# Kernel tuning notes

Hardware: AMD Instinct MI355X
Metric: run time of the kernel (lower is better)

## Reference

```python
import jax, jax.numpy as jnp
import numpy as np
from functools import partial

IMAGE_SIZE = 256
ORIG_SIZE = 1024
NEAR, FAR = 0.1, 100.0
CHUNK = 100  # faces processed per scan step to bound memory


def setup_inputs():
    key = jax.random.key(0)
    kv, kf = jax.random.split(key)
    B, V, F = 4, 5000, 10000
    verts = jax.random.normal(kv, (B, V, 3), jnp.float32) * 0.4
    verts = verts.at[..., 2].add(2.5)  # object in front of camera (+z)
    faces = jax.random.randint(kf, (B, F, 3), 0, V)
    fx = fy = float(ORIG_SIZE)
    cx = cy = ORIG_SIZE / 2.0
    K = jnp.broadcast_to(jnp.array([[fx, 0., cx], [0., fy, cy], [0., 0., 1.]], jnp.float32), (B, 3, 3))
    R = jnp.broadcast_to(jnp.eye(3, dtype=jnp.float32), (B, 3, 3))
    t = jnp.zeros((B, 1, 3), jnp.float32)
    dist_coeffs = jnp.zeros((B, 5), jnp.float32)
    return {"vertices": verts, "faces": faces, "K": K, "R": R, "t": t, "dist_coeffs": dist_coeffs}


def projection(vertices, K, R, t, dist_coeffs, orig_size, eps=1e-9):
    # vertices: [B,V,3]; matmul(vertices, R^T) + t, OpenCV distortion, intrinsics, NDC
    v = jnp.einsum('bvj,bij->bvi', vertices, R) + t
    x, y, z = v[..., 0], v[..., 1], v[..., 2]
    x_ = x / (z + eps)
    y_ = y / (z + eps)
    k1, k2, p1, p2, k3 = [dist_coeffs[:, i:i + 1] for i in range(5)]
    r2 = x_ * x_ + y_ * y_
    rad = 1. + k1 * r2 + k2 * r2 * r2 + k3 * r2 * r2 * r2
    x__ = x_ * rad + 2. * p1 * x_ * y_ + p2 * (r2 + 2. * x_ * x_)
    y__ = y_ * rad + p1 * (r2 + 2. * y_ * y_) + 2. * p2 * x_ * y_
    vv = jnp.stack([x__, y__, jnp.ones_like(z)], axis=-1)
    vv = jnp.einsum('bvj,bij->bvi', vv, K)
    u, vc = vv[..., 0], vv[..., 1]
    vc = orig_size - vc  # image y points down
    u = 2. * (u - orig_size / 2.) / orig_size
    vc = 2. * (vc - orig_size / 2.) / orig_size
    return jnp.stack([u, vc, z], axis=-1)  # [B,V,3] in NDC xy, camera z


def vertices_to_faces(vertices, faces):
    # vertices [B,V,3], faces [B,F,3] -> [B,F,3,3]
    return jnp.take_along_axis(vertices[:, :, None, :], faces[:, :, :, None], axis=1)


def rasterize_depth(face_verts, image_size, near, far):
    # face_verts: [B,F,3,3]; z-buffer min of barycentric-interpolated 1/z depth
    B, F = face_verts.shape[:2]
    pad = (-F) % CHUNK
    fv = jnp.pad(face_verts, ((0, 0), (0, pad), (0, 0), (0, 0)))  # padded faces are degenerate
    n_chunks = (F + pad) // CHUNK
    fv = fv.reshape(B, n_chunks, CHUNK, 3, 3).transpose(1, 0, 2, 3, 4)  # [n,B,C,3,3]
    ps = (2. * jnp.arange(image_size, dtype=jnp.float32) + 1. - image_size) / image_size
    xp = ps[None, None, None, :]  # [1,1,1,W]
    yp = ps[None, None, :, None]  # [1,1,H,1]
    eps = 1e-8

    def step(zbuf, chunk):  # chunk [B,C,3,3]
        x = chunk[..., 0]
        y = chunk[..., 1]
        z = chunk[..., 2]
        x0, x1, x2 = (x[..., i, None, None] for i in range(3))
        y0, y1, y2 = (y[..., i, None, None] for i in range(3))
        z0, z1, z2 = (z[..., i, None, None] for i in range(3))
        denom = (y1 - y2) * (x0 - x2) + (x2 - x1) * (y0 - y2)
        ok = jnp.abs(denom) > eps
        safe_d = jnp.where(ok, denom, 1.)
        w0 = ((y1 - y2) * (xp - x2) + (x2 - x1) * (yp - y2)) / safe_d  # [B,C,H,W]
        w1 = ((y2 - y0) * (xp - x2) + (x0 - x2) * (yp - y2)) / safe_d
        w2 = 1. - w0 - w1
        inside = (w0 >= 0.) & (w1 >= 0.) & (w2 >= 0.) & ok
        zs0 = jnp.where(z0 > eps, z0, 1.)
        zs1 = jnp.where(z1 > eps, z1, 1.)
        zs2 = jnp.where(z2 > eps, z2, 1.)
        zinv = w0 / zs0 + w1 / zs1 + w2 / zs2
        zp = 1. / jnp.where(zinv > eps, zinv, 1.)
        valid = inside & (zp > near) & (zp < far) & (z0 > eps) & (z1 > eps) & (z2 > eps)
        zp = jnp.where(valid, zp, far)
        zbuf = jnp.minimum(zbuf, jnp.min(zp, axis=1))  # min over faces in chunk
        return zbuf, None

    zbuf0 = jnp.full((B, image_size, image_size), far, dtype=face_verts.dtype)
    zbuf, _ = jax.lax.scan(step, zbuf0, fv)
    return zbuf[:, ::-1, :]  # flip vertically to image convention


def reference(vertices, faces, K, R, t, dist_coeffs):
    # fill_back: append faces with reversed winding
    faces_fb = jnp.concatenate([faces, faces[:, :, ::-1]], axis=1)
    v_ndc = projection(vertices, K, R, t, dist_coeffs, float(ORIG_SIZE))
    fverts = vertices_to_faces(v_ndc, faces_fb)  # [B,2F,3,3]
    return rasterize_depth(fverts, IMAGE_SIZE, NEAR, FAR)  # [B,H,W] depth map
```

## Files before the change

kernel.cpp:

```cpp
#include <hip/hip_runtime.h>

#define IMG 256
#define TW 32
#define TH 32
#define TXN (IMG/TW)
#define TYN (IMG/TH)
#define TILES (TXN*TYN)
#define SUBSPLIT 16
#define BIGF 1e30f

typedef float v4f __attribute__((ext_vector_type(4)));

__device__ __forceinline__ float ndc(int i) { return (2.0f*i + 1.0f - IMG) * (1.0f/IMG); }

__device__ __forceinline__ void rank_to_tile(int rank, int& tx, int& ty) {
    int k, base;
    if (rank < 4)       { k = 0; base = 0;  }
    else if (rank < 16) { k = 1; base = 4;  }
    else if (rank < 36) { k = 2; base = 16; }
    else                { k = 3; base = 36; }
    int j = rank - base;
    int s = 2*k + 2;
    int seg = j / (s - 1);
    int off = j - seg * (s - 1);
    int lo = 3 - k, hi = 4 + k;
    if      (seg == 0) { tx = lo + off; ty = lo; }
    else if (seg == 1) { tx = hi;       ty = lo + off; }
    else if (seg == 2) { tx = hi - off; ty = hi; }
    else               { tx = lo;       ty = hi - off; }
}

__global__ void k_prep(const float* __restrict__ verts, const int* __restrict__ faces,
                       const float* __restrict__ Km, const float* __restrict__ Rm,
                       const float* __restrict__ tm, const float* __restrict__ dm,
                       v4f* __restrict__ fd, v4f* __restrict__ bb,
                       unsigned int* __restrict__ outz,
                       int B, int V, int F, int nz, int faceBlocks) {
    if ((int)blockIdx.x >= faceBlocks) {
        int idx = (blockIdx.x - faceBlocks) * 256 + threadIdx.x;
        int stride = (gridDim.x - faceBlocks) * 256;
        for (int j = idx; j < nz; j += stride) outz[j] = 0x42C80000u;
        return;
    }
    int i = blockIdx.x * 256 + threadIdx.x;
    if (i >= B * F) return;
    int b = i / F;
    const float* vb = verts + (size_t)b * V * 3;
    const float* R = Rm + b * 9;
    const float* K = Km + b * 9;
    const float* t = tm + b * 3;
    const float* d = dm + b * 5;
    float X[3], Y[3], Z[3];
    #pragma unroll
    for (int c = 0; c < 3; ++c) {
        int vi = faces[3*i + c];
        float px = vb[3*vi], py = vb[3*vi+1], pz = vb[3*vi+2];
        float x = R[0]*px + R[1]*py + R[2]*pz + t[0];
        float y = R[3]*px + R[4]*py + R[5]*pz + t[1];
        float z = R[6]*px + R[7]*py + R[8]*pz + t[2];
        float iz = 1.0f / (z + 1e-9f);
        float x_ = x * iz, y_ = y * iz;
        float k1 = d[0], k2 = d[1], p1 = d[2], p2 = d[3], k3 = d[4];
        float r2 = x_*x_ + y_*y_;
        float rad = 1.0f + k1*r2 + k2*r2*r2 + k3*r2*r2*r2;
        float xd = x_*rad + 2.0f*p1*x_*y_ + p2*(r2 + 2.0f*x_*x_);
        float yd = y_*rad + p1*(r2 + 2.0f*y_*y_) + 2.0f*p2*x_*y_;
        float u  = K[0]*xd + K[1]*yd + K[2];
        float vc = K[3]*xd + K[4]*yd + K[5];
        vc = 1024.0f - vc;
        X[c] = (u  - 512.0f) * (1.0f/512.0f);
        Y[c] = (vc - 512.0f) * (1.0f/512.0f);
        Z[c] = z;
    }
    float x0=X[0], y0=Y[0], z0=Z[0], x1=X[1], y1=Y[1], z1=Z[1], x2=X[2], y2=Y[2], z2=Z[2];
    float denom = (y1-y2)*(x0-x2) + (x2-x1)*(y0-y2);
    bool ok = (fabsf(denom) > 1e-8f) && (z0 > 1e-8f) && (z1 > 1e-8f) && (z2 > 1e-8f);
    if (!ok) { bb[i] = (v4f){3e38f, -3e38f, 3e38f, -3e38f}; return; }
    float s = (denom > 0.0f) ? 1.0f : -1.0f;
    float absd = fabsf(denom);
    float P0x = s*(y1-y2), P0y = s*(x2-x1);
    float P1x = s*(y2-y0), P1y = s*(x0-x2);
    float P2x = -(P0x + P1x), P2y = -(P0y + P1y);
    float A0 = -(P0x*x2 + P0y*y2);
    float A1 = -(P1x*x2 + P1y*y2);
    float A2 = absd - A0 - A1;
    float ia  = 1.0f / absd;
    float rz0 = ia / z0, rz1 = ia / z1, rz2 = ia / z2;
    float zix = P0x*rz0 + P1x*rz1 + P2x*rz2;
    float ziy = P0y*rz0 + P1y*rz1 + P2y*rz2;
    float zic = A0*rz0 + A1*rz1 + A2*rz2;
    fd[(size_t)i*3 + 0] = (v4f){P0x, P1x, P2x, -zix};
    fd[(size_t)i*3 + 1] = (v4f){P0y, P1y, P2y, -ziy};
    fd[(size_t)i*3 + 2] = (v4f){A0,  A1,  A2,  10.0f - zic};
    bb[i] = (v4f){fminf(x0, fminf(x1, x2)) - 1e-4f,
                  fmaxf(x0, fmaxf(x1, x2)) + 1e-4f,
                  fminf(y0, fminf(y1, y2)) - 1e-4f,
                  fmaxf(y0, fmaxf(y1, y2)) + 1e-4f};
}

__device__ __forceinline__ bool tile_test(v4f gx, v4f gy, v4f a,
                                          float txlo, float txhi, float tylo, float tyhi) {
    float m0 = fmaxf(gx.x*txlo, gx.x*txhi) + fmaxf(gy.x*tylo, gy.x*tyhi) + a.x;
    float m1 = fmaxf(gx.y*txlo, gx.y*txhi) + fmaxf(gy.y*tylo, gy.y*tyhi) + a.y;
    float m2 = fmaxf(gx.z*txlo, gx.z*txhi) + fmaxf(gy.z*tylo, gy.z*tyhi) + a.z;
    return fminf(fminf(m0, m1), m2) >= -1e-5f;
}

__device__ __forceinline__ float plane_min(float gw, float hw, float aw,
                                           float xlo, float xhi, float ylo, float yhi) {
    return fminf(gw*xlo, gw*xhi) + fminf(hw*ylo, hw*yhi) + aw;
}

__device__ __forceinline__ float wave_max_dpp(float v) {
    int x;
    x = __builtin_amdgcn_update_dpp(0, __float_as_int(v), 0x111, 0xF, 0xF, true);
    v = fmaxf(v, __int_as_float(x));
    x = __builtin_amdgcn_update_dpp(0, __float_as_int(v), 0x112, 0xF, 0xF, true);
    v = fmaxf(v, __int_as_float(x));
    x = __builtin_amdgcn_update_dpp(0, __float_as_int(v), 0x114, 0xF, 0xF, true);
    v = fmaxf(v, __int_as_float(x));
    x = __builtin_amdgcn_update_dpp(0, __float_as_int(v), 0x118, 0xF, 0xF, true);
    v = fmaxf(v, __int_as_float(x));
    x = __builtin_amdgcn_update_dpp(0, __float_as_int(v), 0x142, 0xF, 0xF, true);
    v = fmaxf(v, __int_as_float(x));
    x = __builtin_amdgcn_update_dpp(0, __float_as_int(v), 0x143, 0xF, 0xF, true);
    v = fmaxf(v, __int_as_float(x));
    return __int_as_float(__builtin_amdgcn_readlane(__float_as_int(v), 63));
}

__global__ __launch_bounds__(256) void k_raster(const v4f* __restrict__ fd,
                                                const v4f* __restrict__ bb,
                                                unsigned int* __restrict__ outz,
                                                int B, int F) {
    __shared__ v4f sA[257], sB[257], sC[257];
    int tid = threadIdx.x, lane = tid & 63, wave = tid >> 6;
    int wbase = wave << 6;
    int j = blockIdx.x >> 4;
    int s = blockIdx.x & (SUBSPLIT-1);
    int nTB = TILES * B;
    int f_begin = (s * F) / SUBSPLIT, f_end = ((s + 1) * F) / SUBSPLIT;

    #pragma unroll 1
    for (int phase = 0; phase < 2; ++phase) {
        int tb = (phase == 0) ? j : (nTB - 1 - j);
        int rank = tb / B;
        int b = tb - rank * B;
        int tx, ty;
        rank_to_tile(rank, tx, ty);
        int rowbase = ty*TH + wave*8;
        int row = rowbase + (lane >> 3);
        int col = tx*TW + (lane & 7) * 4;
        float yp = ndc(row);
        float xp[4];
        #pragma unroll
        for (int jj = 0; jj < 4; ++jj) xp[jj] = ndc(col + jj);
        float txlo = ndc(tx*TW), txhi = ndc(tx*TW + TW - 1);
        float bylo = ndc(rowbase), byhi = ndc(rowbase + 7);
        float m[4] = {BIGF, BIGF, BIGF, BIGF};
        float h = 9.99f;

        const v4f* bbp = bb + (size_t)b * F;
        const v4f* fdp = fd + (size_t)b * F * 3;

        v4f box = bbp[min(f_begin + lane, f_end - 1)];
        bool valid = (f_begin + lane) < f_end;

        for (int g0 = f_begin; g0 < f_end; g0 += 64) {
            int fn = g0 + 64 + lane;
            v4f nbox = bbp[min(fn, f_end - 1)];
            bool nvalid = fn < f_end;

            bool pass = valid &
                        (box.x <= txhi) & (box.y >= txlo) &
                        (box.z <= byhi) & (box.w >= bylo);
            v4f ra, rb, rc;
            if (pass) {
                int f = g0 + lane;
                ra = fdp[3*f]; rb = fdp[3*f+1]; rc = fdp[3*f+2];
                pass = tile_test(ra, rb, rc, txlo, txhi, bylo, byhi)
                    && (plane_min(ra.w, rb.w, rc.w, txlo, txhi, bylo, byhi) < h);
            }
            unsigned long long mk = __ballot(pass);
            int total = __popcll(mk);
            if (pass) {
                int slot = wbase + __popcll(mk & ((1ull << lane) - 1ull));
                sA[slot] = ra;
                sB[slot] = rb;
                sC[slot] = rc;
            }
            if (total > 0) {
                v4f gx = sA[wbase], gy = sB[wbase], aa = sC[wbase];
                for (int i = 0; i < total; ++i) {
                    v4f nx = sA[wbase+i+1], ny = sB[wbase+i+1], nzv = sC[wbase+i+1];
                    float e0 = fmaf(gy.x, yp, aa.x);
                    float e1 = fmaf(gy.y, yp, aa.y);
                    float e2 = fmaf(gy.z, yp, aa.z);
                    float e3 = fmaf(gy.w, yp, aa.w);
                    #pragma unroll
                    for (int jj = 0; jj < 4; ++jj) {
                        float n0 = fmaf(gx.x, xp[jj], e0);
                        float n1 = fmaf(gx.y, xp[jj], e1);
                        float n2 = fmaf(gx.z, xp[jj], e2);
                        float n3 = fmaf(gx.w, xp[jj], e3);
                        float q = fminf(fminf(n0, n1), n2);
                        m[jj] = fminf(m[jj], (q >= 0.0f) ? n3 : BIGF);
                    }
                    gx = nx; gy = ny; aa = nzv;
                }
                h = fminf(9.99f, wave_max_dpp(fmaxf(fmaxf(m[0], m[1]), fmaxf(m[2], m[3]))));
            }
            box = nbox; valid = nvalid;
        }
        int orow = IMG - 1 - row;
        size_t zo = (size_t)b * (IMG*IMG) + (size_t)orow * IMG + col;
        #pragma unroll
        for (int jj = 0; jj < 4; ++jj) {
            if (m[jj] < 9.99f) {
                float depth = 1.0f / (10.0f - m[jj]);
                unsigned int mv = __float_as_uint(depth);
                unsigned int cv = outz[zo + jj];
                if (mv < cv) atomicMin(&outz[zo + jj], mv);
            }
        }
    }
}

__global__ __launch_bounds__(256) void k_brute(const v4f* __restrict__ fd,
                                               const v4f* __restrict__ bb,
                                               float* __restrict__ out, int B, int F) {
    int bid = blockIdx.x;
    int stripe = bid % 64, b = bid / 64;
    int tid = threadIdx.x, lane = tid & 63, wave = tid >> 6;
    int row = stripe * 4 + wave, colb = lane * 4;
    float yp = ndc(row);
    float xp[4]; float m[4];
    #pragma unroll
    for (int j = 0; j < 4; ++j) { xp[j] = ndc(colb + j); m[j] = BIGF; }
    const v4f* fbb = bb + (size_t)b * F;
    const v4f* ffd = fd + (size_t)b * F * 3;
    for (int f = 0; f < F; ++f) {
        v4f box = fbb[f];
        if (box.z > yp || box.w < yp) continue;
        v4f gx = ffd[3*f], gy = ffd[3*f+1], aa = ffd[3*f+2];
        float e0 = fmaf(gy.x, yp, aa.x);
        float e1 = fmaf(gy.y, yp, aa.y);
        float e2 = fmaf(gy.z, yp, aa.z);
        float e3 = fmaf(gy.w, yp, aa.w);
        #pragma unroll
        for (int j = 0; j < 4; ++j) {
            float n0 = fmaf(gx.x, xp[j], e0);
            float n1 = fmaf(gx.y, xp[j], e1);
            float n2 = fmaf(gx.z, xp[j], e2);
            float n3 = fmaf(gx.w, xp[j], e3);
            float mn = fminf(fminf(fminf(n0, n1), n2), n3);
            m[j] = fminf(m[j], (mn >= 0.0f) ? n3 : BIGF);
        }
    }
    size_t o = (size_t)b*(IMG*IMG) + (size_t)(IMG-1-row)*IMG + colb;
    float4 r;
    r.x = (m[0] < 9.99f) ? 1.0f/(10.0f-m[0]) : 100.0f;
    r.y = (m[1] < 9.99f) ? 1.0f/(10.0f-m[1]) : 100.0f;
    r.z = (m[2] < 9.99f) ? 1.0f/(10.0f-m[2]) : 100.0f;
    r.w = (m[3] < 9.99f) ? 1.0f/(10.0f-m[3]) : 100.0f;
    *(float4*)(out + o) = r;
}

extern "C" void kernel_launch(void* const* d_in, const int* in_sizes, int n_in,
                              void* d_out, int out_size, void* d_ws, size_t ws_size,
                              hipStream_t stream) {
    const float* verts = (const float*)d_in[0];
    const int*   faces = (const int*)d_in[1];
    const float* Km    = (const float*)d_in[2];
    const float* Rm    = (const float*)d_in[3];
    const float* tm    = (const float*)d_in[4];
    const float* dm    = (const float*)d_in[5];
    float* out = (float*)d_out;

    int B = in_sizes[2] / 9;
    int V = in_sizes[0] / (3 * B);
    int F = in_sizes[1] / (3 * B);
    int nz = B * IMG * IMG;

    char* ws = (char*)d_ws;
    size_t al = 255;
    size_t o_fd  = 0;
    size_t o_bb  = (o_fd + (size_t)B*F*48 + al) & ~al;
    size_t need  = o_bb + (size_t)B*F*16;

    v4f* fd  = (v4f*)(ws + o_fd);
    v4f* bbp = (v4f*)(ws + o_bb);

    const int thr = 256;
    int faceBlocks = (B*F + thr - 1) / thr;
    int rasterBlocks = (TILES * B / 2) * SUBSPLIT;
    if (ws_size >= need) {
        k_prep<<<faceBlocks + 128, thr, 0, stream>>>(verts, faces, Km, Rm, tm, dm,
                                                     fd, bbp, (unsigned int*)out,
                                                     B, V, F, nz, faceBlocks);
        k_raster<<<rasterBlocks, thr, 0, stream>>>(fd, bbp, (unsigned int*)out, B, F);
    }
}
```

Before: 139.6 us.

## Use atomic work-ticket queue per wave over tile-band-split items, unroll face loop by two

Replaces the static block-to-tile mapping, where four waves each took one 8-row band of a tile and two phases paired tiles, with a persistent-style dynamic scheduler. Each wave grabs an item (tile, batch, face-split, row band) through a global atomic ticket, so waves balance independently of one another. The face-evaluation inner loop is also unrolled by two, using a sentinel padding entry that can never pass the inside test. This targets load imbalance between center and edge tiles, at the cost of one atomic per item and a ticket reset in the prep kernel.

Result: slower. 363.3 us (+160.1%).

```diff
diff --git a/kernel.cpp b/kernel.cpp
--- a/kernel.cpp
+++ b/kernel.cpp
@@ -34,9 +34,10 @@
                        const float* __restrict__ Km, const float* __restrict__ Rm,
                        const float* __restrict__ tm, const float* __restrict__ dm,
                        v4f* __restrict__ fd, v4f* __restrict__ bb,
-                       unsigned int* __restrict__ outz,
+                       unsigned int* __restrict__ outz, unsigned int* __restrict__ ticket,
                        int B, int V, int F, int nz, int faceBlocks) {
     if ((int)blockIdx.x >= faceBlocks) {
+        if ((int)blockIdx.x == faceBlocks && threadIdx.x == 0) *ticket = 0u;
         int idx = (blockIdx.x - faceBlocks) * 256 + threadIdx.x;
         int stride = (gridDim.x - faceBlocks) * 256;
         for (int j = idx; j < nz; j += stride) outz[j] = 0x42C80000u;
@@ -128,26 +129,46 @@
     return __int_as_float(__builtin_amdgcn_readlane(__float_as_int(v), 63));
 }
 
+#define EVAL_FACE(gx, gy, aa)                                        \
+    {                                                                \
+        float e0 = fmaf((gy).x, yp, (aa).x);                         \
+        float e1 = fmaf((gy).y, yp, (aa).y);                         \
+        float e2 = fmaf((gy).z, yp, (aa).z);                         \
+        float e3 = fmaf((gy).w, yp, (aa).w);                         \
+        _Pragma("unroll")                                            \
+        for (int jj = 0; jj < 4; ++jj) {                             \
+            float n0 = fmaf((gx).x, xp[jj], e0);                     \
+            float n1 = fmaf((gx).y, xp[jj], e1);                     \
+            float n2 = fmaf((gx).z, xp[jj], e2);                     \
+            float n3 = fmaf((gx).w, xp[jj], e3);                     \
+            float q = fminf(fminf(n0, n1), n2);                      \
+            m[jj] = fminf(m[jj], (q >= 0.0f) ? n3 : BIGF);           \
+        }                                                            \
+    }
+
 __global__ __launch_bounds__(256) void k_raster(const v4f* __restrict__ fd,
                                                 const v4f* __restrict__ bb,
                                                 unsigned int* __restrict__ outz,
-                                                int B, int F) {
-    __shared__ v4f sA[257], sB[257], sC[257];
+                                                unsigned int* __restrict__ ticket,
+                                                int B, int F, int nItems) {
+    __shared__ v4f sA[260], sB[260], sC[260];
     int tid = threadIdx.x, lane = tid & 63, wave = tid >> 6;
     int wbase = wave << 6;
-    int j = blockIdx.x >> 4;
-    int s = blockIdx.x & (SUBSPLIT-1);
-    int nTB = TILES * B;
-    int f_begin = (s * F) / SUBSPLIT, f_end = ((s + 1) * F) / SUBSPLIT;
-
-    #pragma unroll 1
-    for (int phase = 0; phase < 2; ++phase) {
-        int tb = (phase == 0) ? j : (nTB - 1 - j);
+
+    for (;;) {
+        int it = 0;
+        if (lane == 0) it = (int)atomicAdd(ticket, 1u);
+        it = __builtin_amdgcn_readfirstlane(it);
+        if (it >= nItems) break;
+
+        int band = it & 3;
+        int sIdx = (it >> 2) & (SUBSPLIT - 1);
+        int tb   = it >> 6;
         int rank = tb / B;
         int b = tb - rank * B;
         int tx, ty;
         rank_to_tile(rank, tx, ty);
-        int rowbase = ty*TH + wave*8;
+        int rowbase = ty*TH + band*8;
         int row = rowbase + (lane >> 3);
         int col = tx*TW + (lane & 7) * 4;
         float yp = ndc(row);
@@ -159,6 +180,7 @@
         float m[4] = {BIGF, BIGF, BIGF, BIGF};
         float h = 9.99f;
 
+        int f_begin = (sIdx * F) / SUBSPLIT, f_end = ((sIdx + 1) * F) / SUBSPLIT;
         const v4f* bbp = bb + (size_t)b * F;
         const v4f* fdp = fd + (size_t)b * F * 3;
 
@@ -189,23 +211,20 @@
                 sC[slot] = rc;
             }
             if (total > 0) {
-                v4f gx = sA[wbase], gy = sB[wbase], aa = sC[wbase];
-                for (int i = 0; i < total; ++i) {
-                    v4f nx = sA[wbase+i+1], ny = sB[wbase+i+1], nzv = sC[wbase+i+1];
-                    float e0 = fmaf(gy.x, yp, aa.x);
-                    float e1 = fmaf(gy.y, yp, aa.y);
-                    float e2 = fmaf(gy.z, yp, aa.z);
-                    float e3 = fmaf(gy.w, yp, aa.w);
-                    #pragma unroll
-                    for (int jj = 0; jj < 4; ++jj) {
-                        float n0 = fmaf(gx.x, xp[jj], e0);
-                        float n1 = fmaf(gx.y, xp[jj], e1);
-                        float n2 = fmaf(gx.z, xp[jj], e2);
-                        float n3 = fmaf(gx.w, xp[jj], e3);
-                        float q = fminf(fminf(n0, n1), n2);
-                        m[jj] = fminf(m[jj], (q >= 0.0f) ? n3 : BIGF);
-                    }
-                    gx = nx; gy = ny; aa = nzv;
+                if (lane == 0) {
+                    sA[wbase+total] = (v4f){0.0f, 0.0f, 0.0f, 0.0f};
+                    sB[wbase+total] = (v4f){0.0f, 0.0f, 0.0f, 0.0f};
+                    sC[wbase+total] = (v4f){-1.0f, -1.0f, -1.0f, 0.0f};
+                }
+                v4f gx0 = sA[wbase+0], gy0 = sB[wbase+0], aa0 = sC[wbase+0];
+                v4f gx1 = sA[wbase+1], gy1 = sB[wbase+1], aa1 = sC[wbase+1];
+                for (int i = 0; i < total; i += 2) {
+                    v4f px0 = sA[wbase+i+2], py0 = sB[wbase+i+2], pa0 = sC[wbase+i+2];
+                    v4f px1 = sA[wbase+i+3], py1 = sB[wbase+i+3], pa1 = sC[wbase+i+3];
+                    EVAL_FACE(gx0, gy0, aa0);
+                    EVAL_FACE(gx1, gy1, aa1);
+                    gx0 = px0; gy0 = py0; aa0 = pa0;
+                    gx1 = px1; gy1 = py1; aa1 = pa1;
                 }
                 h = fminf(9.99f, wave_max_dpp(fmaxf(fmaxf(m[0], m[1]), fmaxf(m[2], m[3]))));
             }
@@ -285,18 +304,22 @@
     size_t al = 255;
     size_t o_fd  = 0;
     size_t o_bb  = (o_fd + (size_t)B*F*48 + al) & ~al;
-    size_t need  = o_bb + (size_t)B*F*16;
+    size_t o_tk  = (o_bb + (size_t)B*F*16 + al) & ~al;
+    size_t need  = o_tk + 256;
 
     v4f* fd  = (v4f*)(ws + o_fd);
     v4f* bbp = (v4f*)(ws + o_bb);
+    unsigned int* ticket = (unsigned int*)(ws + o_tk);
 
     const int thr = 256;
     int faceBlocks = (B*F + thr - 1) / thr;
-    int rasterBlocks = (TILES * B / 2) * SUBSPLIT;
+    int nItems = TILES * B * SUBSPLIT * 4;
+    int rasterBlocks = 2048;
     if (ws_size >= need) {
         k_prep<<<faceBlocks + 128, thr, 0, stream>>>(verts, faces, Km, Rm, tm, dm,
-                                                     fd, bbp, (unsigned int*)out,
+                                                     fd, bbp, (unsigned int*)out, ticket,
                                                      B, V, F, nz, faceBlocks);
-        k_raster<<<rasterBlocks, thr, 0, stream>>>(fd, bbp, (unsigned int*)out, B, F);
-    }
-}
+        k_raster<<<rasterBlocks, thr, 0, stream>>>(fd, bbp, (unsigned int*)out, ticket,
+                                                   B, F, nItems);
+    }
+}
```

## Bin faces into per-tile lists before rasterizing instead of scanning all faces

Applied to the files above, without the earlier changes.

Adds a binning pipeline in place of scanning every face per tile. k_prep computes a per-face tile coverage mask and per-bin counts, k_scan builds prefix offsets, and k_fill writes face ids into per-(tile,batch) lists. k_raster then walks only its bin's ids, split across the subsplit blocks. This removes the cost of each tile iterating over all faces, at the price of three extra launches, a memset, a second coverage computation, atomics, and indirect gathers through the id list. The old full-scan raster is kept as a fallback when the workspace is too small.

Result: slower. 157.6 us (+12.8%).

```diff
diff --git a/kernel.cpp b/kernel.cpp
--- a/kernel.cpp
+++ b/kernel.cpp
@@ -3,9 +3,9 @@
 #define IMG 256
 #define TW 32
 #define TH 32
-#define TXN (IMG/TW)
-#define TYN (IMG/TH)
-#define TILES (TXN*TYN)
+#define TXN 8
+#define TYN 8
+#define TILES 64
 #define SUBSPLIT 16
 #define BIGF 1e30f
 
@@ -30,74 +30,6 @@
     else               { tx = lo;       ty = hi - off; }
 }
 
-__global__ void k_prep(const float* __restrict__ verts, const int* __restrict__ faces,
-                       const float* __restrict__ Km, const float* __restrict__ Rm,
-                       const float* __restrict__ tm, const float* __restrict__ dm,
-                       v4f* __restrict__ fd, v4f* __restrict__ bb,
-                       unsigned int* __restrict__ outz,
-                       int B, int V, int F, int nz, int faceBlocks) {
-    if ((int)blockIdx.x >= faceBlocks) {
-        int idx = (blockIdx.x - faceBlocks) * 256 + threadIdx.x;
-        int stride = (gridDim.x - faceBlocks) * 256;
-        for (int j = idx; j < nz; j += stride) outz[j] = 0x42C80000u;
-        return;
-    }
-    int i = blockIdx.x * 256 + threadIdx.x;
-    if (i >= B * F) return;
-    int b = i / F;
-    const float* vb = verts + (size_t)b * V * 3;
-    const float* R = Rm + b * 9;
-    const float* K = Km + b * 9;
-    const float* t = tm + b * 3;
-    const float* d = dm + b * 5;
-    float X[3], Y[3], Z[3];
-    #pragma unroll
-    for (int c = 0; c < 3; ++c) {
-        int vi = faces[3*i + c];
-        float px = vb[3*vi], py = vb[3*vi+1], pz = vb[3*vi+2];
-        float x = R[0]*px + R[1]*py + R[2]*pz + t[0];
-        float y = R[3]*px + R[4]*py + R[5]*pz + t[1];
-        float z = R[6]*px + R[7]*py + R[8]*pz + t[2];
-        float iz = 1.0f / (z + 1e-9f);
-        float x_ = x * iz, y_ = y * iz;
-        float k1 = d[0], k2 = d[1], p1 = d[2], p2 = d[3], k3 = d[4];
-        float r2 = x_*x_ + y_*y_;
-        float rad = 1.0f + k1*r2 + k2*r2*r2 + k3*r2*r2*r2;
-        float xd = x_*rad + 2.0f*p1*x_*y_ + p2*(r2 + 2.0f*x_*x_);
-        float yd = y_*rad + p1*(r2 + 2.0f*y_*y_) + 2.0f*p2*x_*y_;
-        float u  = K[0]*xd + K[1]*yd + K[2];
-        float vc = K[3]*xd + K[4]*yd + K[5];
-        vc = 1024.0f - vc;
-        X[c] = (u  - 512.0f) * (1.0f/512.0f);
-        Y[c] = (vc - 512.0f) * (1.0f/512.0f);
-        Z[c] = z;
-    }
-    float x0=X[0], y0=Y[0], z0=Z[0], x1=X[1], y1=Y[1], z1=Z[1], x2=X[2], y2=Y[2], z2=Z[2];
-    float denom = (y1-y2)*(x0-x2) + (x2-x1)*(y0-y2);
-    bool ok = (fabsf(denom) > 1e-8f) && (z0 > 1e-8f) && (z1 > 1e-8f) && (z2 > 1e-8f);
-    if (!ok) { bb[i] = (v4f){3e38f, -3e38f, 3e38f, -3e38f}; return; }
-    float s = (denom > 0.0f) ? 1.0f : -1.0f;
-    float absd = fabsf(denom);
-    float P0x = s*(y1-y2), P0y = s*(x2-x1);
-    float P1x = s*(y2-y0), P1y = s*(x0-x2);
-    float P2x = -(P0x + P1x), P2y = -(P0y + P1y);
-    float A0 = -(P0x*x2 + P0y*y2);
-    float A1 = -(P1x*x2 + P1y*y2);
-    float A2 = absd - A0 - A1;
-    float ia  = 1.0f / absd;
-    float rz0 = ia / z0, rz1 = ia / z1, rz2 = ia / z2;
-    float zix = P0x*rz0 + P1x*rz1 + P2x*rz2;
-    float ziy = P0y*rz0 + P1y*rz1 + P2y*rz2;
-    float zic = A0*rz0 + A1*rz1 + A2*rz2;
-    fd[(size_t)i*3 + 0] = (v4f){P0x, P1x, P2x, -zix};
-    fd[(size_t)i*3 + 1] = (v4f){P0y, P1y, P2y, -ziy};
-    fd[(size_t)i*3 + 2] = (v4f){A0,  A1,  A2,  10.0f - zic};
-    bb[i] = (v4f){fminf(x0, fminf(x1, x2)) - 1e-4f,
-                  fmaxf(x0, fmaxf(x1, x2)) + 1e-4f,
-                  fminf(y0, fminf(y1, y2)) - 1e-4f,
-                  fmaxf(y0, fmaxf(y1, y2)) + 1e-4f};
-}
-
 __device__ __forceinline__ bool tile_test(v4f gx, v4f gy, v4f a,
                                           float txlo, float txhi, float tylo, float tyhi) {
     float m0 = fmaxf(gx.x*txlo, gx.x*txhi) + fmaxf(gy.x*tylo, gy.x*tyhi) + a.x;
@@ -128,10 +60,303 @@
     return __int_as_float(__builtin_amdgcn_readlane(__float_as_int(v), 63));
 }
 
+__device__ __forceinline__ unsigned long long cover_mask(float xmn, float xmx,
+                                                         float ymn, float ymx,
+                                                         v4f gx, v4f gy, v4f aa) {
+    int i0 = (int)floorf(xmn*128.0f + 127.5f);
+    int i1 = (int)ceilf (xmx*128.0f + 127.5f);
+    int j0 = (int)floorf(ymn*128.0f + 127.5f);
+    int j1 = (int)ceilf (ymx*128.0f + 127.5f);
+    if (i0 > 255 || i1 < 0 || j0 > 255 || j1 < 0) return 0ull;
+    int tx0 = max(i0, 0) >> 5, tx1 = min(i1, 255) >> 5;
+    int ty0 = max(j0, 0) >> 5, ty1 = min(j1, 255) >> 5;
+    unsigned long long m = 0ull;
+    for (int ty = ty0; ty <= ty1; ++ty) {
+        float tylo = ndc(ty*TH), tyhi = ndc(ty*TH + TH - 1);
+        for (int tx = tx0; tx <= tx1; ++tx) {
+            if (tile_test(gx, gy, aa, ndc(tx*TW), ndc(tx*TW + TW - 1), tylo, tyhi))
+                m |= 1ull << (ty*8 + tx);
+        }
+    }
+    return m;
+}
+
+__global__ void k_prep(const float* __restrict__ verts, const int* __restrict__ faces,
+                       const float* __restrict__ Km, const float* __restrict__ Rm,
+                       const float* __restrict__ tm, const float* __restrict__ dm,
+                       v4f* __restrict__ fd, v4f* __restrict__ bb,
+                       unsigned int* __restrict__ outz, unsigned int* __restrict__ gcnt,
+                       int B, int V, int F, int nz, int faceBlocks, int doBins) {
+    if ((int)blockIdx.x >= faceBlocks) {
+        int idx = (blockIdx.x - faceBlocks) * 256 + threadIdx.x;
+        int stride = (gridDim.x - faceBlocks) * 256;
+        for (int j = idx; j < nz; j += stride) outz[j] = 0x42C80000u;
+        return;
+    }
+    __shared__ int lcnt[1024];
+    int nbins = TILES * B;
+    int tid = threadIdx.x;
+    if (doBins) {
+        for (int k = tid; k < nbins; k += 256) lcnt[k] = 0;
+        __syncthreads();
+    }
+    int i = blockIdx.x * 256 + tid;
+    bool alive = i < B * F;
+    unsigned long long tmask = 0ull;
+    int b = 0;
+    if (alive) {
+        b = i / F;
+        const float* vb = verts + (size_t)b * V * 3;
+        const float* R = Rm + b * 9;
+        const float* K = Km + b * 9;
+        const float* t = tm + b * 3;
+        const float* d = dm + b * 5;
+        float X[3], Y[3], Z[3];
+        #pragma unroll
+        for (int c = 0; c < 3; ++c) {
+            int vi = faces[3*i + c];
+            float px = vb[3*vi], py = vb[3*vi+1], pz = vb[3*vi+2];
+            float x = R[0]*px + R[1]*py + R[2]*pz + t[0];
+            float y = R[3]*px + R[4]*py + R[5]*pz + t[1];
+            float z = R[6]*px + R[7]*py + R[8]*pz + t[2];
+            float iz = 1.0f / (z + 1e-9f);
+            float x_ = x * iz, y_ = y * iz;
+            float k1 = d[0], k2 = d[1], p1 = d[2], p2 = d[3], k3 = d[4];
+            float r2 = x_*x_ + y_*y_;
+            float rad = 1.0f + k1*r2 + k2*r2*r2 + k3*r2*r2*r2;
+            float xd = x_*rad + 2.0f*p1*x_*y_ + p2*(r2 + 2.0f*x_*x_);
+            float yd = y_*rad + p1*(r2 + 2.0f*y_*y_) + 2.0f*p2*x_*y_;
+            float u  = K[0]*xd + K[1]*yd + K[2];
+            float vc = K[3]*xd + K[4]*yd + K[5];
+            vc = 1024.0f - vc;
+            X[c] = (u  - 512.0f) * (1.0f/512.0f);
+            Y[c] = (vc - 512.0f) * (1.0f/512.0f);
+            Z[c] = z;
+        }
+        float x0=X[0], y0=Y[0], z0=Z[0], x1=X[1], y1=Y[1], z1=Z[1], x2=X[2], y2=Y[2], z2=Z[2];
+        float denom = (y1-y2)*(x0-x2) + (x2-x1)*(y0-y2);
+        bool ok = (fabsf(denom) > 1e-8f) && (z0 > 1e-8f) && (z1 > 1e-8f) && (z2 > 1e-8f);
+        if (!ok) {
+            bb[i] = (v4f){3e38f, -3e38f, 3e38f, -3e38f};
+        } else {
+            float s = (denom > 0.0f) ? 1.0f : -1.0f;
+            float absd = fabsf(denom);
+            float P0x = s*(y1-y2), P0y = s*(x2-x1);
+            float P1x = s*(y2-y0), P1y = s*(x0-x2);
+            float P2x = -(P0x + P1x), P2y = -(P0y + P1y);
+            float A0 = -(P0x*x2 + P0y*y2);
+            float A1 = -(P1x*x2 + P1y*y2);
+            float A2 = absd - A0 - A1;
+            float ia  = 1.0f / absd;
+            float rz0 = ia / z0, rz1 = ia / z1, rz2 = ia / z2;
+            float zix = P0x*rz0 + P1x*rz1 + P2x*rz2;
+            float ziy = P0y*rz0 + P1y*rz1 + P2y*rz2;
+            float zic = A0*rz0 + A1*rz1 + A2*rz2;
+            v4f ga = (v4f){P0x, P1x, P2x, -zix};
+            v4f gb = (v4f){P0y, P1y, P2y, -ziy};
+            v4f gc = (v4f){A0,  A1,  A2,  10.0f - zic};
+            fd[(size_t)i*3 + 0] = ga;
+            fd[(size_t)i*3 + 1] = gb;
+            fd[(size_t)i*3 + 2] = gc;
+            float xmn = fminf(x0, fminf(x1, x2)) - 1e-4f;
+            float xmx = fmaxf(x0, fmaxf(x1, x2)) + 1e-4f;
+            float ymn = fminf(y0, fminf(y1, y2)) - 1e-4f;
+            float ymx = fmaxf(y0, fmaxf(y1, y2)) + 1e-4f;
+            bb[i] = (v4f){xmn, xmx, ymn, ymx};
+            if (doBins) tmask = cover_mask(xmn, xmx, ymn, ymx, ga, gb, gc);
+        }
+    }
+    if (doBins) {
+        unsigned long long mk = tmask;
+        while (mk) {
+            int t = __builtin_ctzll(mk); mk &= mk - 1ull;
+            atomicAdd(&lcnt[t*B + b], 1);
+        }
+        __syncthreads();
+        for (int k = tid; k < nbins; k += 256)
+            if (lcnt[k]) atomicAdd(&gcnt[k], (unsigned int)lcnt[k]);
+    }
+}
+
+__global__ __launch_bounds__(256) void k_scan(const unsigned int* __restrict__ gcnt,
+                                              unsigned int* __restrict__ goff,
+                                              unsigned int* __restrict__ gcur, int nbins) {
+    __shared__ unsigned int ps[256];
+    int tid = threadIdx.x;
+    unsigned int loc[4], s = 0;
+    #pragma unroll
+    for (int k = 0; k < 4; ++k) {
+        int idx = tid*4 + k;
+        unsigned int c = (idx < nbins) ? gcnt[idx] : 0u;
+        loc[k] = c; s += c;
+    }
+    ps[tid] = s; __syncthreads();
+    #pragma unroll
+    for (int d = 1; d < 256; d <<= 1) {
+        unsigned int t = (tid >= d) ? ps[tid - d] : 0u;
+        __syncthreads();
+        ps[tid] += t;
+        __syncthreads();
+    }
+    unsigned int run = ps[tid] - s;
+    #pragma unroll
+    for (int k = 0; k < 4; ++k) {
+        int idx = tid*4 + k;
+        if (idx < nbins) {
+            goff[idx] = run; gcur[idx] = run; run += loc[k];
+            if (idx == nbins - 1) goff[nbins] = run;
+        }
+    }
+}
+
+__global__ void k_fill(const v4f* __restrict__ fd, const v4f* __restrict__ bb,
+                       unsigned int* __restrict__ gcur, unsigned int* __restrict__ ids,
+                       int B, int F) {
+    __shared__ int lcnt[1024];
+    __shared__ unsigned int lbase[1024];
+    __shared__ int lofs[1024];
+    int nbins = TILES * B;
+    int tid = threadIdx.x;
+    for (int k = tid; k < nbins; k += 256) { lcnt[k] = 0; lofs[k] = 0; }
+    __syncthreads();
+    int i = blockIdx.x * 256 + tid;
+    bool alive = i < B * F;
+    unsigned long long tmask = 0ull;
+    int b = 0;
+    if (alive) {
+        b = i / F;
+        v4f box = bb[i];
+        if (box.x <= box.y) {
+            v4f ga = fd[(size_t)i*3], gb = fd[(size_t)i*3+1], gc = fd[(size_t)i*3+2];
+            tmask = cover_mask(box.x, box.y, box.z, box.w, ga, gb, gc);
+        }
+    }
+    unsigned long long mk = tmask;
+    while (mk) {
+        int t = __builtin_ctzll(mk); mk &= mk - 1ull;
+        atomicAdd(&lcnt[t*B + b], 1);
+    }
+    __syncthreads();
+    for (int k = tid; k < nbins; k += 256)
+        if (lcnt[k]) lbase[k] = atomicAdd(&gcur[k], (unsigned int)lcnt[k]);
+    __syncthreads();
+    mk = tmask;
+    while (mk) {
+        int t = __builtin_ctzll(mk); mk &= mk - 1ull;
+        int bin = t*B + b;
+        int sl = atomicAdd(&lofs[bin], 1);
+        ids[lbase[bin] + sl] = (unsigned int)i;
+    }
+}
+
 __global__ __launch_bounds__(256) void k_raster(const v4f* __restrict__ fd,
                                                 const v4f* __restrict__ bb,
+                                                const unsigned int* __restrict__ ids,
+                                                const unsigned int* __restrict__ goff,
+                                                const unsigned int* __restrict__ gcnt,
                                                 unsigned int* __restrict__ outz,
                                                 int B, int F) {
+    __shared__ v4f sA[260], sB[260], sC[260];
+    int tid = threadIdx.x, lane = tid & 63, wave = tid >> 6;
+    int wbase = wave << 6;
+    int j = blockIdx.x >> 4;
+    int s = blockIdx.x & (SUBSPLIT-1);
+    int nTB = TILES * B;
+
+    #pragma unroll 1
+    for (int phase = 0; phase < 2; ++phase) {
+        int tb = (phase == 0) ? j : (nTB - 1 - j);
+        int rank = tb / B;
+        int b = tb - rank * B;
+        int tx, ty;
+        rank_to_tile(rank, tx, ty);
+        int bin = (ty*8 + tx)*B + b;
+        unsigned int off = goff[bin], len = gcnt[bin];
+        unsigned int p0 = off + (unsigned int)(( (unsigned long long)s    * len) / SUBSPLIT);
+        unsigned int p1 = off + (unsigned int)(( (unsigned long long)(s+1)* len) / SUBSPLIT);
+
+        int rowbase = ty*TH + wave*8;
+        int row = rowbase + (lane >> 3);
+        int col = tx*TW + (lane & 7) * 4;
+        float yp = ndc(row);
+        float xp[4];
+        #pragma unroll
+        for (int jj = 0; jj < 4; ++jj) xp[jj] = ndc(col + jj);
+        float txlo = ndc(tx*TW), txhi = ndc(tx*TW + TW - 1);
+        float bylo = ndc(rowbase), byhi = ndc(rowbase + 7);
+        float m[4] = {BIGF, BIGF, BIGF, BIGF};
+        float h = 9.99f;
+
+        if (p1 > p0) {
+            unsigned int idc = ids[min(p0 + lane, p1 - 1)];
+            bool vc = (p0 + lane) < p1;
+            v4f boxc = bb[idc];
+            unsigned int idn = ids[min(p0 + 64 + lane, p1 - 1)];
+            bool vn = (p0 + 64 + lane) < p1;
+
+            for (unsigned int p = p0; p < p1; p += 64) {
+                v4f boxn = bb[idn];
+                unsigned int id2 = ids[min(p + 128 + lane, p1 - 1)];
+                bool v2 = (p + 128 + lane) < p1;
+
+                bool pass = vc & (boxc.z <= byhi) & (boxc.w >= bylo);
+                v4f ra, rb, rc;
+                if (pass) {
+                    ra = fd[(size_t)idc*3]; rb = fd[(size_t)idc*3+1]; rc = fd[(size_t)idc*3+2];
+                    pass = tile_test(ra, rb, rc, txlo, txhi, bylo, byhi)
+                        && (plane_min(ra.w, rb.w, rc.w, txlo, txhi, bylo, byhi) < h);
+                }
+                unsigned long long mk = __ballot(pass);
+                int total = __popcll(mk);
+                if (pass) {
+                    int slot = wbase + __popcll(mk & ((1ull << lane) - 1ull));
+                    sA[slot] = ra;
+                    sB[slot] = rb;
+                    sC[slot] = rc;
+                }
+                if (total > 0) {
+                    v4f gx = sA[wbase], gy = sB[wbase], aa = sC[wbase];
+                    for (int i = 0; i < total; ++i) {
+                        v4f nx = sA[wbase+i+1], ny = sB[wbase+i+1], nzv = sC[wbase+i+1];
+                        float e0 = fmaf(gy.x, yp, aa.x);
+                        float e1 = fmaf(gy.y, yp, aa.y);
+                        float e2 = fmaf(gy.z, yp, aa.z);
+                        float e3 = fmaf(gy.w, yp, aa.w);
+                        #pragma unroll
+                        for (int jj = 0; jj < 4; ++jj) {
+                            float n0 = fmaf(gx.x, xp[jj], e0);
+                            float n1 = fmaf(gx.y, xp[jj], e1);
+                            float n2 = fmaf(gx.z, xp[jj], e2);
+                            float n3 = fmaf(gx.w, xp[jj], e3);
+                            float q = fminf(fminf(n0, n1), n2);
+                            m[jj] = fminf(m[jj], (q >= 0.0f) ? n3 : BIGF);
+                        }
+                        gx = nx; gy = ny; aa = nzv;
+                    }
+                    h = fminf(9.99f, wave_max_dpp(fmaxf(fmaxf(m[0], m[1]), fmaxf(m[2], m[3]))));
+                }
+                idc = idn; boxc = boxn; vc = vn;
+                idn = id2; vn = v2;
+            }
+        }
+        int orow = IMG - 1 - row;
+        size_t zo = (size_t)b * (IMG*IMG) + (size_t)orow * IMG + col;
+        #pragma unroll
+        for (int jj = 0; jj < 4; ++jj) {
+            if (m[jj] < 9.99f) {
+                float depth = 1.0f / (10.0f - m[jj]);
+                unsigned int mv = __float_as_uint(depth);
+                unsigned int cv = outz[zo + jj];
+                if (mv < cv) atomicMin(&outz[zo + jj], mv);
+            }
+        }
+    }
+}
+
+__global__ __launch_bounds__(256) void k_raster_scan(const v4f* __restrict__ fd,
+                                                     const v4f* __restrict__ bb,
+                                                     unsigned int* __restrict__ outz,
+                                                     int B, int F) {
     __shared__ v4f sA[257], sB[257], sC[257];
     int tid = threadIdx.x, lane = tid & 63, wave = tid >> 6;
     int wbase = wave << 6;
@@ -225,46 +450,6 @@
     }
 }
 
-__global__ __launch_bounds__(256) void k_brute(const v4f* __restrict__ fd,
-                                               const v4f* __restrict__ bb,
-                                               float* __restrict__ out, int B, int F) {
-    int bid = blockIdx.x;
-    int stripe = bid % 64, b = bid / 64;
-    int tid = threadIdx.x, lane = tid & 63, wave = tid >> 6;
-    int row = stripe * 4 + wave, colb = lane * 4;
-    float yp = ndc(row);
-    float xp[4]; float m[4];
-    #pragma unroll
-    for (int j = 0; j < 4; ++j) { xp[j] = ndc(colb + j); m[j] = BIGF; }
-    const v4f* fbb = bb + (size_t)b * F;
-    const v4f* ffd = fd + (size_t)b * F * 3;
-    for (int f = 0; f < F; ++f) {
-        v4f box = fbb[f];
-        if (box.z > yp || box.w < yp) continue;
-        v4f gx = ffd[3*f], gy = ffd[3*f+1], aa = ffd[3*f+2];
-        float e0 = fmaf(gy.x, yp, aa.x);
-        float e1 = fmaf(gy.y, yp, aa.y);
-        float e2 = fmaf(gy.z, yp, aa.z);
-        float e3 = fmaf(gy.w, yp, aa.w);
-        #pragma unroll
-        for (int j = 0; j < 4; ++j) {
-            float n0 = fmaf(gx.x, xp[j], e0);
-            float n1 = fmaf(gx.y, xp[j], e1);
-            float n2 = fmaf(gx.z, xp[j], e2);
-            float n3 = fmaf(gx.w, xp[j], e3);
-            float mn = fminf(fminf(fminf(n0, n1), n2), n3);
-            m[j] = fminf(m[j], (mn >= 0.0f) ? n3 : BIGF);
-        }
-    }
-    size_t o = (size_t)b*(IMG*IMG) + (size_t)(IMG-1-row)*IMG + colb;
-    float4 r;
-    r.x = (m[0] < 9.99f) ? 1.0f/(10.0f-m[0]) : 100.0f;
-    r.y = (m[1] < 9.99f) ? 1.0f/(10.0f-m[1]) : 100.0f;
-    r.z = (m[2] < 9.99f) ? 1.0f/(10.0f-m[2]) : 100.0f;
-    r.w = (m[3] < 9.99f) ? 1.0f/(10.0f-m[3]) : 100.0f;
-    *(float4*)(out + o) = r;
-}
-
 extern "C" void kernel_launch(void* const* d_in, const int* in_sizes, int n_in,
                               void* d_out, int out_size, void* d_ws, size_t ws_size,
                               hipStream_t stream) {
@@ -280,23 +465,43 @@
     int V = in_sizes[0] / (3 * B);
     int F = in_sizes[1] / (3 * B);
     int nz = B * IMG * IMG;
+    int nbins = TILES * B;
 
     char* ws = (char*)d_ws;
     size_t al = 255;
     size_t o_fd  = 0;
     size_t o_bb  = (o_fd + (size_t)B*F*48 + al) & ~al;
-    size_t need  = o_bb + (size_t)B*F*16;
+    size_t o_cnt = (o_bb + (size_t)B*F*16 + al) & ~al;
+    size_t o_cur = (o_cnt + (size_t)nbins*4 + al) & ~al;
+    size_t o_off = (o_cur + (size_t)nbins*4 + al) & ~al;
+    size_t o_ids = (o_off + (size_t)(nbins+1)*4 + al) & ~al;
+    size_t need_bins = o_ids + (size_t)B*F*64*4;
+    size_t need_scan = o_cnt;
 
     v4f* fd  = (v4f*)(ws + o_fd);
     v4f* bbp = (v4f*)(ws + o_bb);
+    unsigned int* gcnt = (unsigned int*)(ws + o_cnt);
+    unsigned int* gcur = (unsigned int*)(ws + o_cur);
+    unsigned int* goff = (unsigned int*)(ws + o_off);
+    unsigned int* ids  = (unsigned int*)(ws + o_ids);
 
     const int thr = 256;
     int faceBlocks = (B*F + thr - 1) / thr;
     int rasterBlocks = (TILES * B / 2) * SUBSPLIT;
-    if (ws_size >= need) {
+
+    if (ws_size >= need_bins && nbins <= 1024) {
+        hipMemsetAsync(gcnt, 0, (size_t)nbins*4, stream);
         k_prep<<<faceBlocks + 128, thr, 0, stream>>>(verts, faces, Km, Rm, tm, dm,
-                                                     fd, bbp, (unsigned int*)out,
-                                                     B, V, F, nz, faceBlocks);
-        k_raster<<<rasterBlocks, thr, 0, stream>>>(fd, bbp, (unsigned int*)out, B, F);
-    }
-}
+                                                     fd, bbp, (unsigned int*)out, gcnt,
+                                                     B, V, F, nz, faceBlocks, 1);
+        k_scan<<<1, thr, 0, stream>>>(gcnt, goff, gcur, nbins);
+        k_fill<<<faceBlocks, thr, 0, stream>>>(fd, bbp, gcur, ids, B, F);
+        k_raster<<<rasterBlocks, thr, 0, stream>>>(fd, bbp, ids, goff, gcnt,
+                                                   (unsigned int*)out, B, F);
+    } else if (ws_size >= need_scan) {
+        k_prep<<<faceBlocks + 128, thr, 0, stream>>>(verts, faces, Km, Rm, tm, dm,
+                                                     fd, bbp, (unsigned int*)out, gcnt,
+                                                     B, V, F, nz, faceBlocks, 0);
+        k_raster_scan<<<rasterBlocks, thr, 0, stream>>>(fd, bbp, (unsigned int*)out, B, F);
+    }
+}
```
